# Kernel tuning notes

Measured on AMD Instinct MI355X. Metric: run time of the kernel, lower is better.

Reference implementation:

```python
import jax, jax.numpy as jnp
import numpy as np

B, DIM, H, W = 4, 512, 64, 64
HEADS = 8
MAX_FREQ = 10000.0


def _rope_cos_sin(h, w, head_dim, dtype):
    # 2D RoPE: first quarter of half_dim uses row position, second quarter uses col position
    half = head_dim // 2
    quarter = half // 2
    pos_h = jnp.arange(h, dtype=dtype)
    pos_w = jnp.arange(w, dtype=dtype)
    gh, gw = jnp.meshgrid(pos_h, pos_w, indexing='ij')
    pos = jnp.stack([gh.ravel(), gw.ravel()], axis=-1)  # [N, 2]
    freqs = 1.0 / (MAX_FREQ ** (jnp.arange(quarter, dtype=dtype) / quarter))  # [quarter]
    ang_x = pos[:, 0:1] * freqs  # [N, quarter]
    ang_y = pos[:, 1:2] * freqs  # [N, quarter]
    cos = jnp.concatenate([jnp.cos(ang_x), jnp.cos(ang_y)], axis=-1)  # [N, half]
    sin = jnp.concatenate([jnp.sin(ang_x), jnp.sin(ang_y)], axis=-1)  # [N, half]
    return cos, sin


def _apply_rope(x, cos, sin):
    # x: [B, heads, N, head_dim]; cos/sin: [N, head_dim//2]
    d = x.shape[-1] // 2
    x1, x2 = x[..., :d], x[..., d:]
    return jnp.concatenate([x1 * cos - x2 * sin, x1 * sin + x2 * cos], axis=-1)


def setup_inputs() -> dict:
    key = jax.random.key(0)
    kx, kq, kp = jax.random.split(key, 3)
    x = jax.random.normal(kx, (B, DIM, H, W), dtype=jnp.float32)
    w_qkv = jax.random.normal(kq, (3 * DIM, DIM), dtype=jnp.float32) * (DIM ** -0.5)
    w_proj = jax.random.normal(kp, (DIM, DIM), dtype=jnp.float32) * (DIM ** -0.5)
    return {"x": x, "w_qkv": w_qkv, "w_proj": w_proj}


def reference(x, w_qkv, w_proj):
    Bb, C, Hh, Ww = x.shape
    heads = HEADS
    hd = C // heads
    N = Hh * Ww
    # 1x1 conv (bias-free) == channel-wise linear
    qkv = jnp.einsum('bchw,oc->bohw', x, w_qkv)  # [B, 3C, H, W]
    qkv = qkv.reshape(Bb, 3, heads, hd, Hh, Ww).transpose(1, 0, 2, 4, 5, 3)  # [3, B, heads, H, W, hd]
    q = qkv[0].reshape(Bb, heads, N, hd)
    k = qkv[1].reshape(Bb, heads, N, hd)
    v = qkv[2].reshape(Bb, heads, N, hd)
    cos, sin = _rope_cos_sin(Hh, Ww, hd, x.dtype)
    q = _apply_rope(q, cos, sin)
    k = _apply_rope(k, cos, sin)
    scale = hd ** -0.5
    attn = jax.nn.softmax(jnp.einsum('bhnd,bhmd->bhnm', q, k) * scale, axis=-1)  # [B, heads, N, N]
    out = jnp.einsum('bhnm,bhmd->bhnd', attn, v)  # [B, heads, N, hd]
    out = out.reshape(Bb, heads, Hh, Ww, hd).transpose(0, 1, 4, 2, 3).reshape(Bb, C, Hh, Ww)
    return jnp.einsum('bchw,oc->bohw', out, w_proj)
```

## Files before the change

### kernel.cpp

```cpp
#include <hip/hip_runtime.h>
#include <math.h>

#define B_    4
#define CDIM  512
#define HEADS 8
#define HD    64
#define NN    4096
#define QSZ   ((size_t)B_*HEADS*NN*HD)
#define SCALE_Q 0.18033688011112042f

typedef __attribute__((ext_vector_type(8))) short short8;
typedef __attribute__((ext_vector_type(4))) float f32x4;
union U4S8 { uint4 u; short8 s; };

__device__ inline unsigned pk(float a, float b) {
    unsigned ua = __float_as_uint(a), ub = __float_as_uint(b);
    ua += 0x7FFFu + ((ua >> 16) & 1u);
    ub += 0x7FFFu + ((ub >> 16) & 1u);
    return (ua >> 16) | (ub & 0xFFFF0000u);
}
__device__ inline unsigned short bf16_1(float a) {
    unsigned ua = __float_as_uint(a);
    ua += 0x7FFFu + ((ua >> 16) & 1u);
    return (unsigned short)(ua >> 16);
}
__device__ inline unsigned pkru(float a, float b) {
    unsigned ua = __float_as_uint(a) + 0x8000u;
    unsigned ub = __float_as_uint(b) + 0x8000u;
    return __builtin_amdgcn_perm(ub, ua, 0x07060302);
}

__device__ inline void load_lds16(const unsigned short* g, unsigned short* l) {
    __builtin_amdgcn_global_load_lds(
        (const __attribute__((address_space(1))) unsigned int*)g,
        (__attribute__((address_space(3))) unsigned int*)l, 16, 0, 0);
}

__global__ void conv_w_kernel(const float* __restrict__ wq, const float* __restrict__ wp,
                              unsigned short* __restrict__ wqb, unsigned short* __restrict__ wpb) {
    int id = blockIdx.x * 256 + threadIdx.x;
    const float* src; unsigned short* dst; size_t off; float sc = 1.0f;
    if (id < 98304) { src = wq; dst = wqb; off = (size_t)id * 8; if (off < 262144) sc = SCALE_Q; }
    else            { src = wp; dst = wpb; off = (size_t)(id - 98304) * 8; }
    float4 a = *(const float4*)(src + off);
    float4 b = *(const float4*)(src + off + 4);
    uint4 u;
    u.x = pk(a.x * sc, a.y * sc); u.y = pk(a.z * sc, a.w * sc);
    u.z = pk(b.x * sc, b.y * sc); u.w = pk(b.z * sc, b.w * sc);
    *(uint4*)(dst + off) = u;
}

__global__ void rope_table_kernel(float* __restrict__ ct, float* __restrict__ st) {
    int id = blockIdx.x * 256 + threadIdx.x;
    int j = id >> 12, n = id & 4095;
    int i = j & 15;
    float pos = (j < 16) ? (float)(n >> 6) : (float)(n & 63);
    float freq = exp2f(-(float)i * 0.8304820237218406f);
    float ang = pos * freq;
    ct[id] = cosf(ang);
    st[id] = sinf(ang);
}

__global__ __launch_bounds__(256) void transpose_x_kernel(
        const float* __restrict__ x, unsigned short* __restrict__ xt) {
    __shared__ unsigned short T[64 * 72];
    int t = threadIdx.x;
    int b = blockIdx.z, c0 = blockIdx.y * 64, n0 = blockIdx.x * 64;
    const float* xb = x + ((size_t)b * CDIM + c0) * NN + n0;
    int crow = t >> 2, nseg = t & 3;
#pragma unroll
    for (int g = 0; g < 4; ++g) {
        float4 f = *(const float4*)(xb + (size_t)crow * NN + nseg * 16 + g * 4);
        int nb = nseg * 16 + g * 4;
        T[(nb + 0) * 72 + crow] = bf16_1(f.x);
        T[(nb + 1) * 72 + crow] = bf16_1(f.y);
        T[(nb + 2) * 72 + crow] = bf16_1(f.z);
        T[(nb + 3) * 72 + crow] = bf16_1(f.w);
    }
    __syncthreads();
    unsigned short* xo = xt + ((size_t)b * NN + n0) * CDIM + c0;
    int nrow = t >> 2, cseg = t & 3;
    uint4 u0 = *(uint4*)(T + nrow * 72 + cseg * 16);
    uint4 u1 = *(uint4*)(T + nrow * 72 + cseg * 16 + 8);
    *(uint4*)(xo + (size_t)nrow * CDIM + cseg * 16)     = u0;
    *(uint4*)(xo + (size_t)nrow * CDIM + cseg * 16 + 8) = u1;
}

__global__ __launch_bounds__(256, 2) void qkv_mfma_kernel(
        const unsigned short* __restrict__ xt, const unsigned short* __restrict__ wq,
        unsigned short* __restrict__ qbf, unsigned short* __restrict__ kbf,
        unsigned short* __restrict__ vt,
        const float* __restrict__ ct, const float* __restrict__ st) {
    __shared__ unsigned short smem[8192];
    int t = threadIdx.x;
    int lane = t & 63, w = t >> 6;
    int qlo = lane & 15, quad = lane >> 4;
    int b = blockIdx.z, o0 = blockIdx.y * 128, n0 = blockIdx.x * 128;
    const unsigned short* xb = xt + (size_t)b * NN * CDIM;
    int row = t >> 2, seg = t & 3;
    int wn = (w & 1) * 64, wo = (w >> 1) * 64;

    f32x4 acc[4][4];
#pragma unroll
    for (int i = 0; i < 4; ++i)
#pragma unroll
        for (int j = 0; j < 4; ++j) acc[i][j] = f32x4{0.f, 0.f, 0.f, 0.f};

    for (int k0 = 0; k0 < 512; k0 += 32) {
        __syncthreads();
        load_lds16(xb + (size_t)(n0 + row) * 512 + k0 + seg * 8,        smem + t * 8);
        load_lds16(xb + (size_t)(n0 + 64 + row) * 512 + k0 + seg * 8,   smem + 2048 + t * 8);
        load_lds16(wq + (size_t)(o0 + row) * 512 + k0 + seg * 8,        smem + 4096 + t * 8);
        load_lds16(wq + (size_t)(o0 + 64 + row) * 512 + k0 + seg * 8,   smem + 6144 + t * 8);
        __syncthreads();
        U4S8 af[4], bf[4];
#pragma unroll
        for (int mt = 0; mt < 4; ++mt)
            af[mt].u = *(const uint4*)(smem + (wn + 16 * mt + qlo) * 32 + quad * 8);
#pragma unroll
        for (int nt = 0; nt < 4; ++nt)
            bf[nt].u = *(const uint4*)(smem + 4096 + (wo + 16 * nt + qlo) * 32 + quad * 8);
#pragma unroll
        for (int mt = 0; mt < 4; ++mt)
#pragma unroll
            for (int nt = 0; nt < 4; ++nt)
                acc[mt][nt] = __builtin_amdgcn_mfma_f32_16x16x32_bf16(
                    af[mt].s, bf[nt].s, acc[mt][nt], 0, 0, 0);
    }

    int og = o0 + wo;
    int s = og >> 9;
    int h = (og & 511) >> 6;
    int bh = b * HEADS + h;
    if (s < 2) {
        unsigned short* dst = (s ? kbf : qbf) + (size_t)bh * NN * HD;
#pragma unroll
        for (int mt = 0; mt < 4; ++mt) {
            int nbase = n0 + wn + 16 * mt + 4 * quad;
#pragma unroll
            for (int ntp = 0; ntp < 2; ++ntp) {
                int j = 16 * ntp + qlo;
                float4 c4 = *(const float4*)(ct + (size_t)j * NN + nbase);
                float4 s4 = *(const float4*)(st + (size_t)j * NN + nbase);
                float cc[4] = {c4.x, c4.y, c4.z, c4.w};
                float ss[4] = {s4.x, s4.y, s4.z, s4.w};
#pragma unroll
                for (int r = 0; r < 4; ++r) {
                    float x1 = acc[mt][ntp][r], x2 = acc[mt][ntp + 2][r];
                    size_t base = (size_t)(nbase + r) * HD;
                    dst[base + j]      = bf16_1(x1 * cc[r] - x2 * ss[r]);
                    dst[base + j + 32] = bf16_1(x1 * ss[r] + x2 * cc[r]);
                }
            }
        }
    } else {
        unsigned short* dst = vt + (size_t)bh * HD * NN;
#pragma unroll
        for (int mt = 0; mt < 4; ++mt)
#pragma unroll
            for (int nt = 0; nt < 4; ++nt) {
                int d = 16 * nt + qlo;
                int n = n0 + wn + 16 * mt + 4 * quad;
                uint2 u;
                u.x = pk(acc[mt][nt][0], acc[mt][nt][1]);
                u.y = pk(acc[mt][nt][2], acc[mt][nt][3]);
                *(uint2*)(dst + (size_t)d * NN + n) = u;
            }
    }
}

__global__ __launch_bounds__(256, 2) void attn_kernel(
        const unsigned short* __restrict__ qbf, const unsigned short* __restrict__ kbf,
        const unsigned short* __restrict__ vt, unsigned short* __restrict__ aot) {
    __shared__ unsigned char smem[18432];
    int t = threadIdx.x;
    int lane = t & 63, w = t >> 6;
    int qlo = lane & 15, quad = lane >> 4;
    int bb = blockIdx.z, hh = blockIdx.y;
    int bh = bb * HEADS + hh;
    int n0w = blockIdx.x * 256 + w * 64;

    U4S8 qf[4][2];
    const unsigned short* qg = qbf + ((size_t)bh * NN + n0w) * HD;
#pragma unroll
    for (int nt = 0; nt < 4; ++nt)
#pragma unroll
        for (int kt = 0; kt < 2; ++kt)
            qf[nt][kt].u = *(const uint4*)(qg + (size_t)(16 * nt + qlo) * 64 + 32 * kt + 8 * quad);

    f32x4 O[4][4];
#pragma unroll
    for (int mt = 0; mt < 4; ++mt)
#pragma unroll
        for (int nt = 0; nt < 4; ++nt) O[mt][nt] = f32x4{0.f, 0.f, 0.f, 0.f};
    float lx[4] = {0.f, 0.f, 0.f, 0.f};
    float ly[4] = {0.f, 0.f, 0.f, 0.f};

    const uint4* kg = (const uint4*)kbf + (size_t)bh * NN * 8;
    const uint4* vg = (const uint4*)vt  + (size_t)bh * 64 * 512;

    int rr0 = t >> 3, s8 = t & 7;
    int voff = (s8 >> 2) * 64 + (s8 & 1) * 32 + ((s8 >> 1) & 1) * 8;
    uint4 kr0, kr1, vr0, vr1;
    kr0 = kg[(size_t)rr0 * 8 + s8];
    kr1 = kg[(size_t)(32 + rr0) * 8 + s8];
    vr0 = vg[(size_t)rr0 * 512 + s8];
    vr1 = vg[(size_t)(32 + rr0) * 512 + s8];

    for (int c = 0; c < NN / 64; ++c) {
        __syncthreads();
        *(uint4*)(smem + rr0 * 144 + s8 * 16)        = kr0;
        *(uint4*)(smem + (32 + rr0) * 144 + s8 * 16) = kr1;
        *(uint2*)(smem + 9216 + rr0 * 144 + voff)            = make_uint2(vr0.x, vr0.y);
        *(uint2*)(smem + 9216 + rr0 * 144 + voff + 16)       = make_uint2(vr0.z, vr0.w);
        *(uint2*)(smem + 9216 + (32 + rr0) * 144 + voff)     = make_uint2(vr1.x, vr1.y);
        *(uint2*)(smem + 9216 + (32 + rr0) * 144 + voff + 16)= make_uint2(vr1.z, vr1.w);
        __syncthreads();
        if (c + 1 < NN / 64) {
            int m0 = (c + 1) * 64;
            kr0 = kg[(size_t)(m0 + rr0) * 8 + s8];
            kr1 = kg[(size_t)(m0 + 32 + rr0) * 8 + s8];
            vr0 = vg[(size_t)rr0 * 512 + (m0 >> 3) + s8];
            vr1 = vg[(size_t)(32 + rr0) * 512 + (m0 >> 3) + s8];
        }

        f32x4 S[4][4];
#pragma unroll
        for (int mt = 0; mt < 4; ++mt)
#pragma unroll
            for (int nt = 0; nt < 4; ++nt) S[mt][nt] = f32x4{0.f, 0.f, 0.f, 0.f};
#pragma unroll
        for (int kt = 0; kt < 2; ++kt) {
            U4S8 ka[4];
#pragma unroll
            for (int mt = 0; mt < 4; ++mt)
                ka[mt].u = *(const uint4*)(smem + (16 * mt + qlo) * 144 + kt * 64 + quad * 16);
#pragma unroll
            for (int nt = 0; nt < 4; ++nt)
#pragma unroll
                for (int mt = 0; mt < 4; ++mt)
                    S[mt][nt] = __builtin_amdgcn_mfma_f32_16x16x32_bf16(
                        ka[mt].s, qf[nt][kt].s, S[mt][nt], 0, 0, 0);
        }

        uint2 pd[4][4];
#pragma unroll
        for (int nt = 0; nt < 4; ++nt)
#pragma unroll
            for (int mt = 0; mt < 4; ++mt) {
                f32x4 s4 = S[mt][nt];
                float p0 = __builtin_amdgcn_exp2f(s4[0]);
                float p1 = __builtin_amdgcn_exp2f(s4[1]);
                float p2 = __builtin_amdgcn_exp2f(s4[2]);
                float p3 = __builtin_amdgcn_exp2f(s4[3]);
                lx[nt] += p0 + p2;
                ly[nt] += p1 + p3;
                pd[nt][mt] = make_uint2(pkru(p0, p1), pkru(p2, p3));
            }

#pragma unroll
        for (int kt = 0; kt < 2; ++kt) {
            U4S8 pa[4];
#pragma unroll
            for (int mtP = 0; mtP < 4; ++mtP)
                pa[mtP].u = make_uint4(pd[mtP][2 * kt].x, pd[mtP][2 * kt].y,
                                       pd[mtP][2 * kt + 1].x, pd[mtP][2 * kt + 1].y);
#pragma unroll
            for (int nt = 0; nt < 4; ++nt) {
                U4S8 vb;
                vb.u = *(const uint4*)(smem + 9216 + (16 * nt + qlo) * 144 + kt * 64 + quad * 16);
#pragma unroll
                for (int mtP = 0; mtP < 4; ++mtP)
                    O[mtP][nt] = __builtin_amdgcn_mfma_f32_16x16x32_bf16(
                        pa[mtP].s, vb.s, O[mtP][nt], 0, 0, 0);
            }
        }
    }

    float linv[4];
#pragma unroll
    for (int nt = 0; nt < 4; ++nt) {
        float l = lx[nt] + ly[nt];
        l += __shfl_xor(l, 16, 64);
        l += __shfl_xor(l, 32, 64);
        linv[nt] = 1.0f / l;
    }
    __syncthreads();
    unsigned short* Tw = (unsigned short*)(smem + w * 4608);
    unsigned short* aob = aot + ((size_t)bb * NN) * CDIM + hh * 64;
#pragma unroll
    for (int mt = 0; mt < 4; ++mt) {
        float iv[4];
#pragma unroll
        for (int r = 0; r < 4; ++r) iv[r] = __shfl(linv[mt], 4 * quad + r, 64);
#pragma unroll
        for (int nt = 0; nt < 4; ++nt)
#pragma unroll
            for (int r = 0; r < 4; ++r)
                Tw[(4 * quad + r) * 72 + 16 * nt + qlo] = bf16_1(O[mt][nt][r] * iv[r]);
        int row = lane >> 2, cseg = lane & 3;
        uint4 u0 = *(uint4*)(Tw + row * 72 + cseg * 16);
        uint4 u1 = *(uint4*)(Tw + row * 72 + cseg * 16 + 8);
        unsigned short* arow = aob + (size_t)(n0w + 16 * mt + row) * CDIM + cseg * 16;
        *(uint4*)(arow)     = u0;
        *(uint4*)(arow + 8) = u1;
    }
}

__global__ __launch_bounds__(256, 2) void proj_mfma_kernel(
        const unsigned short* __restrict__ aot, const unsigned short* __restrict__ wp,
        float* __restrict__ out) {
    __shared__ unsigned short smem[8192];
    int t = threadIdx.x;
    int lane = t & 63, w = t >> 6;
    int qlo = lane & 15, quad = lane >> 4;
    int b = blockIdx.z, o0 = blockIdx.y * 128, n0 = blockIdx.x * 128;
    const unsigned short* ab = aot + (size_t)b * NN * CDIM;
    int row = t >> 2, seg = t & 3;
    int wn = (w & 1) * 64, wo = (w >> 1) * 64;

    f32x4 acc[4][4];
#pragma unroll
    for (int i = 0; i < 4; ++i)
#pragma unroll
        for (int j = 0; j < 4; ++j) acc[i][j] = f32x4{0.f, 0.f, 0.f, 0.f};

    for (int k0 = 0; k0 < 512; k0 += 32) {
        __syncthreads();
        load_lds16(ab + (size_t)(n0 + row) * 512 + k0 + seg * 8,        smem + t * 8);
        load_lds16(ab + (size_t)(n0 + 64 + row) * 512 + k0 + seg * 8,   smem + 2048 + t * 8);
        load_lds16(wp + (size_t)(o0 + row) * 512 + k0 + seg * 8,        smem + 4096 + t * 8);
        load_lds16(wp + (size_t)(o0 + 64 + row) * 512 + k0 + seg * 8,   smem + 6144 + t * 8);
        __syncthreads();
        U4S8 af[4], bf[4];
#pragma unroll
        for (int mt = 0; mt < 4; ++mt)
            af[mt].u = *(const uint4*)(smem + (wn + 16 * mt + qlo) * 32 + quad * 8);
#pragma unroll
        for (int nt = 0; nt < 4; ++nt)
            bf[nt].u = *(const uint4*)(smem + 4096 + (wo + 16 * nt + qlo) * 32 + quad * 8);
#pragma unroll
        for (int mt = 0; mt < 4; ++mt)
#pragma unroll
            for (int nt = 0; nt < 4; ++nt)
                acc[mt][nt] = __builtin_amdgcn_mfma_f32_16x16x32_bf16(
                    af[mt].s, bf[nt].s, acc[mt][nt], 0, 0, 0);
    }

    float* ob = out + (size_t)b * CDIM * NN;
#pragma unroll
    for (int mt = 0; mt < 4; ++mt)
#pragma unroll
        for (int nt = 0; nt < 4; ++nt) {
            int o = o0 + wo + 16 * nt + qlo;
            int n = n0 + wn + 16 * mt + 4 * quad;
            *(float4*)(ob + (size_t)o * NN + n) = *(float4*)&acc[mt][nt];
        }
}

extern "C" void kernel_launch(void* const* d_in, const int* in_sizes, int n_in,
                              void* d_out, int out_size, void* d_ws, size_t ws_size,
                              hipStream_t stream) {
    const float* x      = (const float*)d_in[0];
    const float* w_qkv  = (const float*)d_in[1];
    const float* w_proj = (const float*)d_in[2];
    float* out = (float*)d_out;
    unsigned short* ws = (unsigned short*)d_ws;

    unsigned short* xt  = ws;
    unsigned short* qbf = xt  + QSZ;
    unsigned short* kbf = qbf + QSZ;
    unsigned short* vt  = kbf + QSZ;
    unsigned short* aot = vt  + QSZ;
    unsigned short* wqb = aot + QSZ;
    unsigned short* wpb = wqb + 786432;
    float* ct = (float*)(wpb + 262144);
    float* st = ct + 32 * 4096;

    conv_w_kernel<<<512, 256, 0, stream>>>(w_qkv, w_proj, wqb, wpb);
    rope_table_kernel<<<512, 256, 0, stream>>>(ct, st);
    transpose_x_kernel<<<dim3(64, 8, B_), 256, 0, stream>>>(x, xt);
    qkv_mfma_kernel<<<dim3(32, 12, B_), 256, 0, stream>>>(xt, wqb, qbf, kbf, vt, ct, st);
    attn_kernel<<<dim3(NN / 256, HEADS, B_), 256, 0, stream>>>(qbf, kbf, vt, aot);
    proj_mfma_kernel<<<dim3(32, 4, B_), 256, 0, stream>>>(aot, wpb, out);
}
```

Before: 291.6 us.

## Rewrite attention inner loop with 32x32x16 MFMA, 128-key tiles and MFMA row sums

The attention kernel switches from 16x16x32 to 32x32x16 bf16 MFMA tiles and stages 128 keys per iteration instead of 64, which halves the number of barriers. The softmax denominator is now accumulated by an extra MFMA against a ones vector rather than scalar adds and cross-lane shuffles. The grid becomes 1D with a remapped block index so that blocks sharing the same head are scheduled close together, which may improve L2 reuse of K and V. In exchange, LDS use roughly doubles, register pressure rises from the 16-wide accumulators, and the extra MFMAs for the row sums add matrix-unit work.

```diff
diff --git a/kernel.cpp b/kernel.cpp
--- a/kernel.cpp
+++ b/kernel.cpp
@@ -11,6 +11,7 @@
 
 typedef __attribute__((ext_vector_type(8))) short short8;
 typedef __attribute__((ext_vector_type(4))) float f32x4;
+typedef __attribute__((ext_vector_type(16))) float f32x16;
 union U4S8 { uint4 u; short8 s; };
 
 __device__ inline unsigned pk(float a, float b) {
@@ -172,138 +173,135 @@
 __global__ __launch_bounds__(256, 2) void attn_kernel(
         const unsigned short* __restrict__ qbf, const unsigned short* __restrict__ kbf,
         const unsigned short* __restrict__ vt, unsigned short* __restrict__ aot) {
-    __shared__ unsigned char smem[18432];
+    __shared__ unsigned char smem[35840];
+    const int VB = 18432;
     int t = threadIdx.x;
     int lane = t & 63, w = t >> 6;
-    int qlo = lane & 15, quad = lane >> 4;
-    int bb = blockIdx.z, hh = blockIdx.y;
-    int bh = bb * HEADS + hh;
-    int n0w = blockIdx.x * 256 + w * 64;
-
-    U4S8 qf[4][2];
+    int lo5 = lane & 31, h = lane >> 5;
+    int L = blockIdx.x;
+    int bh = (L & 7) + 8 * (L >> 7);
+    int qb = (L >> 3) & 15;
+    int bb = bh >> 3, hh = bh & 7;
+    int n0w = qb * 256 + w * 64;
+
+    U4S8 qf[2][4];
     const unsigned short* qg = qbf + ((size_t)bh * NN + n0w) * HD;
 #pragma unroll
-    for (int nt = 0; nt < 4; ++nt)
-#pragma unroll
-        for (int kt = 0; kt < 2; ++kt)
-            qf[nt][kt].u = *(const uint4*)(qg + (size_t)(16 * nt + qlo) * 64 + 32 * kt + 8 * quad);
-
-    f32x4 O[4][4];
-#pragma unroll
-    for (int mt = 0; mt < 4; ++mt)
-#pragma unroll
-        for (int nt = 0; nt < 4; ++nt) O[mt][nt] = f32x4{0.f, 0.f, 0.f, 0.f};
-    float lx[4] = {0.f, 0.f, 0.f, 0.f};
-    float ly[4] = {0.f, 0.f, 0.f, 0.f};
+    for (int qt = 0; qt < 2; ++qt)
+#pragma unroll
+        for (int kt = 0; kt < 4; ++kt)
+            qf[qt][kt].u = *(const uint4*)(qg + (size_t)(32 * qt + lo5) * 64 + kt * 16 + 8 * h);
+
+    f32x16 O[2][2], lac[2];
+#pragma unroll
+    for (int i = 0; i < 16; ++i) {
+        O[0][0][i] = 0.f; O[0][1][i] = 0.f; O[1][0][i] = 0.f; O[1][1][i] = 0.f;
+        lac[0][i] = 0.f; lac[1][i] = 0.f;
+    }
+    U4S8 ones;
+    ones.u = make_uint4(0x3F803F80u, 0x3F803F80u, 0x3F803F80u, 0x3F803F80u);
 
     const uint4* kg = (const uint4*)kbf + (size_t)bh * NN * 8;
     const uint4* vg = (const uint4*)vt  + (size_t)bh * 64 * 512;
 
-    int rr0 = t >> 3, s8 = t & 7;
-    int voff = (s8 >> 2) * 64 + (s8 & 1) * 32 + ((s8 >> 1) & 1) * 8;
-    uint4 kr0, kr1, vr0, vr1;
-    kr0 = kg[(size_t)rr0 * 8 + s8];
-    kr1 = kg[(size_t)(32 + rr0) * 8 + s8];
-    vr0 = vg[(size_t)rr0 * 512 + s8];
-    vr1 = vg[(size_t)(32 + rr0) * 512 + s8];
-
-    for (int c = 0; c < NN / 64; ++c) {
-        __syncthreads();
-        *(uint4*)(smem + rr0 * 144 + s8 * 16)        = kr0;
-        *(uint4*)(smem + (32 + rr0) * 144 + s8 * 16) = kr1;
-        *(uint2*)(smem + 9216 + rr0 * 144 + voff)            = make_uint2(vr0.x, vr0.y);
-        *(uint2*)(smem + 9216 + rr0 * 144 + voff + 16)       = make_uint2(vr0.z, vr0.w);
-        *(uint2*)(smem + 9216 + (32 + rr0) * 144 + voff)     = make_uint2(vr1.x, vr1.y);
-        *(uint2*)(smem + 9216 + (32 + rr0) * 144 + voff + 16)= make_uint2(vr1.z, vr1.w);
-        __syncthreads();
-        if (c + 1 < NN / 64) {
-            int m0 = (c + 1) * 64;
-            kr0 = kg[(size_t)(m0 + rr0) * 8 + s8];
-            kr1 = kg[(size_t)(m0 + 32 + rr0) * 8 + s8];
-            vr0 = vg[(size_t)rr0 * 512 + (m0 >> 3) + s8];
-            vr1 = vg[(size_t)(32 + rr0) * 512 + (m0 >> 3) + s8];
-        }
-
-        f32x4 S[4][4];
-#pragma unroll
-        for (int mt = 0; mt < 4; ++mt)
-#pragma unroll
-            for (int nt = 0; nt < 4; ++nt) S[mt][nt] = f32x4{0.f, 0.f, 0.f, 0.f};
-#pragma unroll
-        for (int kt = 0; kt < 2; ++kt) {
-            U4S8 ka[4];
-#pragma unroll
-            for (int mt = 0; mt < 4; ++mt)
-                ka[mt].u = *(const uint4*)(smem + (16 * mt + qlo) * 144 + kt * 64 + quad * 16);
-#pragma unroll
-            for (int nt = 0; nt < 4; ++nt)
-#pragma unroll
-                for (int mt = 0; mt < 4; ++mt)
-                    S[mt][nt] = __builtin_amdgcn_mfma_f32_16x16x32_bf16(
-                        ka[mt].s, qf[nt][kt].s, S[mt][nt], 0, 0, 0);
-        }
-
-        uint2 pd[4][4];
-#pragma unroll
-        for (int nt = 0; nt < 4; ++nt)
-#pragma unroll
-            for (int mt = 0; mt < 4; ++mt) {
-                f32x4 s4 = S[mt][nt];
-                float p0 = __builtin_amdgcn_exp2f(s4[0]);
-                float p1 = __builtin_amdgcn_exp2f(s4[1]);
-                float p2 = __builtin_amdgcn_exp2f(s4[2]);
-                float p3 = __builtin_amdgcn_exp2f(s4[3]);
-                lx[nt] += p0 + p2;
-                ly[nt] += p1 + p3;
-                pd[nt][mt] = make_uint2(pkru(p0, p1), pkru(p2, p3));
-            }
-
-#pragma unroll
-        for (int kt = 0; kt < 2; ++kt) {
-            U4S8 pa[4];
-#pragma unroll
-            for (int mtP = 0; mtP < 4; ++mtP)
-                pa[mtP].u = make_uint4(pd[mtP][2 * kt].x, pd[mtP][2 * kt].y,
-                                       pd[mtP][2 * kt + 1].x, pd[mtP][2 * kt + 1].y);
-#pragma unroll
-            for (int nt = 0; nt < 4; ++nt) {
-                U4S8 vb;
-                vb.u = *(const uint4*)(smem + 9216 + (16 * nt + qlo) * 144 + kt * 64 + quad * 16);
-#pragma unroll
-                for (int mtP = 0; mtP < 4; ++mtP)
-                    O[mtP][nt] = __builtin_amdgcn_mfma_f32_16x16x32_bf16(
-                        pa[mtP].s, vb.s, O[mtP][nt], 0, 0, 0);
-            }
-        }
-    }
-
-    float linv[4];
-#pragma unroll
-    for (int nt = 0; nt < 4; ++nt) {
-        float l = lx[nt] + ly[nt];
-        l += __shfl_xor(l, 16, 64);
-        l += __shfl_xor(l, 32, 64);
-        linv[nt] = 1.0f / l;
-    }
+    int kof[4], vof[4];
+    const uint4* kgp[4]; const uint4* vgp[4];
+    uint4 kr[4], vr[4];
+#pragma unroll
+    for (int i = 0; i < 4; ++i) {
+        int idx = t + 256 * i;
+        kof[i] = (idx >> 3) * 144 + (idx & 7) * 16;
+        kgp[i] = kg + (size_t)(idx >> 3) * 8 + (idx & 7);
+        int hd = idx >> 4, u = idx & 15;
+        vof[i] = VB + hd * 272 + 32 * (u >> 1) + 8 * (u & 1);
+        vgp[i] = vg + (size_t)hd * 512 + u;
+        kr[i] = kgp[i][0];
+        vr[i] = vgp[i][0];
+    }
+
+    for (int it = 0; it < 32; ++it) {
+        __syncthreads();
+#pragma unroll
+        for (int i = 0; i < 4; ++i)
+            *(uint4*)(smem + kof[i]) = kr[i];
+#pragma unroll
+        for (int i = 0; i < 4; ++i) {
+            *(uint2*)(smem + vof[i])      = make_uint2(vr[i].x, vr[i].y);
+            *(uint2*)(smem + vof[i] + 16) = make_uint2(vr[i].z, vr[i].w);
+        }
+        __syncthreads();
+        if (it + 1 < 32) {
+#pragma unroll
+            for (int i = 0; i < 4; ++i) {
+                kr[i] = kgp[i][(size_t)(it + 1) * 1024];
+                vr[i] = vgp[i][(size_t)(it + 1) * 16];
+            }
+        }
+
+#pragma unroll
+        for (int sc = 0; sc < 2; ++sc) {
+            U4S8 pa[2][4];
+#pragma unroll
+            for (int mt = 0; mt < 2; ++mt) {
+                f32x16 S0 = {0.f,0.f,0.f,0.f,0.f,0.f,0.f,0.f,0.f,0.f,0.f,0.f,0.f,0.f,0.f,0.f};
+                f32x16 S1 = {0.f,0.f,0.f,0.f,0.f,0.f,0.f,0.f,0.f,0.f,0.f,0.f,0.f,0.f,0.f,0.f};
+                int kbase = 9216 * sc + 4608 * mt + lo5 * 144 + 16 * h;
+#pragma unroll
+                for (int kt = 0; kt < 4; ++kt) {
+                    U4S8 ka;
+                    ka.u = *(const uint4*)(smem + kbase + kt * 32);
+                    S0 = __builtin_amdgcn_mfma_f32_32x32x16_bf16(ka.s, qf[0][kt].s, S0, 0, 0, 0);
+                    S1 = __builtin_amdgcn_mfma_f32_32x32x16_bf16(ka.s, qf[1][kt].s, S1, 0, 0, 0);
+                }
+#pragma unroll
+                for (int gg = 0; gg < 2; ++gg) {
+                    int rb = 8 * gg;
+                    pa[0][2 * mt + gg].u = make_uint4(
+                        pkru(__builtin_amdgcn_exp2f(S0[rb + 0]), __builtin_amdgcn_exp2f(S0[rb + 1])),
+                        pkru(__builtin_amdgcn_exp2f(S0[rb + 2]), __builtin_amdgcn_exp2f(S0[rb + 3])),
+                        pkru(__builtin_amdgcn_exp2f(S0[rb + 4]), __builtin_amdgcn_exp2f(S0[rb + 5])),
+                        pkru(__builtin_amdgcn_exp2f(S0[rb + 6]), __builtin_amdgcn_exp2f(S0[rb + 7])));
+                    pa[1][2 * mt + gg].u = make_uint4(
+                        pkru(__builtin_amdgcn_exp2f(S1[rb + 0]), __builtin_amdgcn_exp2f(S1[rb + 1])),
+                        pkru(__builtin_amdgcn_exp2f(S1[rb + 2]), __builtin_amdgcn_exp2f(S1[rb + 3])),
+                        pkru(__builtin_amdgcn_exp2f(S1[rb + 4]), __builtin_amdgcn_exp2f(S1[rb + 5])),
+                        pkru(__builtin_amdgcn_exp2f(S1[rb + 6]), __builtin_amdgcn_exp2f(S1[rb + 7])));
+                }
+            }
+            int vbase = VB + lo5 * 272 + 16 * h + 128 * sc;
+#pragma unroll
+            for (int g = 0; g < 4; ++g) {
+                U4S8 vb0, vb1;
+                vb0.u = *(const uint4*)(smem + vbase + 32 * g);
+                vb1.u = *(const uint4*)(smem + vbase + 8704 + 32 * g);
+                lac[0]  = __builtin_amdgcn_mfma_f32_32x32x16_bf16(pa[0][g].s, ones.s, lac[0], 0, 0, 0);
+                lac[1]  = __builtin_amdgcn_mfma_f32_32x32x16_bf16(pa[1][g].s, ones.s, lac[1], 0, 0, 0);
+                O[0][0] = __builtin_amdgcn_mfma_f32_32x32x16_bf16(pa[0][g].s, vb0.s, O[0][0], 0, 0, 0);
+                O[0][1] = __builtin_amdgcn_mfma_f32_32x32x16_bf16(pa[0][g].s, vb1.s, O[0][1], 0, 0, 0);
+                O[1][0] = __builtin_amdgcn_mfma_f32_32x32x16_bf16(pa[1][g].s, vb0.s, O[1][0], 0, 0, 0);
+                O[1][1] = __builtin_amdgcn_mfma_f32_32x32x16_bf16(pa[1][g].s, vb1.s, O[1][1], 0, 0, 0);
+            }
+        }
+    }
+
     __syncthreads();
     unsigned short* Tw = (unsigned short*)(smem + w * 4608);
-    unsigned short* aob = aot + ((size_t)bb * NN) * CDIM + hh * 64;
-#pragma unroll
-    for (int mt = 0; mt < 4; ++mt) {
-        float iv[4];
-#pragma unroll
-        for (int r = 0; r < 4; ++r) iv[r] = __shfl(linv[mt], 4 * quad + r, 64);
-#pragma unroll
-        for (int nt = 0; nt < 4; ++nt)
-#pragma unroll
-            for (int r = 0; r < 4; ++r)
-                Tw[(4 * quad + r) * 72 + 16 * nt + qlo] = bf16_1(O[mt][nt][r] * iv[r]);
-        int row = lane >> 2, cseg = lane & 3;
-        uint4 u0 = *(uint4*)(Tw + row * 72 + cseg * 16);
-        uint4 u1 = *(uint4*)(Tw + row * 72 + cseg * 16 + 8);
-        unsigned short* arow = aob + (size_t)(n0w + 16 * mt + row) * CDIM + cseg * 16;
-        *(uint4*)(arow)     = u0;
-        *(uint4*)(arow + 8) = u1;
+    unsigned short* aob = aot + (size_t)bb * NN * CDIM + hh * 64;
+#pragma unroll
+    for (int qt = 0; qt < 2; ++qt) {
+#pragma unroll
+        for (int r = 0; r < 16; ++r) {
+            int qrow = (r & 3) + 8 * (r >> 2) + 4 * h;
+            float inv = __builtin_amdgcn_rcpf(lac[qt][r]);
+            Tw[qrow * 68 + lo5]      = bf16_1(O[qt][0][r] * inv);
+            Tw[qrow * 68 + 32 + lo5] = bf16_1(O[qt][1][r] * inv);
+        }
+        unsigned short* arow = aob + (size_t)(n0w + 32 * qt + (lane >> 1)) * CDIM + (lane & 1) * 8;
+#pragma unroll
+        for (int rep = 0; rep < 4; ++rep) {
+            uint4 u = *(const uint4*)(Tw + (lane >> 1) * 68 + (lane & 1) * 8 + rep * 16);
+            *(uint4*)(arow + rep * 16) = u;
+        }
     }
 }
 
@@ -381,6 +379,6 @@
     rope_table_kernel<<<512, 256, 0, stream>>>(ct, st);
     transpose_x_kernel<<<dim3(64, 8, B_), 256, 0, stream>>>(x, xt);
     qkv_mfma_kernel<<<dim3(32, 12, B_), 256, 0, stream>>>(xt, wqb, qbf, kbf, vt, ct, st);
-    attn_kernel<<<dim3(NN / 256, HEADS, B_), 256, 0, stream>>>(qbf, kbf, vt, aot);
+    attn_kernel<<<512, 256, 0, stream>>>(qbf, kbf, vt, aot);
     proj_mfma_kernel<<<dim3(32, 4, B_), 256, 0, stream>>>(aot, wpb, out);
 }
```

Result: slower. 319.1 us (+9.4%).

## Halve attention query tile per block and remap grid for more blocks

Applied to the files above, without the earlier changes.

The attention kernel now gives each block 128 queries (32 per wave) instead of 256, which doubles the grid to 1024 blocks, and raises the launch-bounds occupancy hint from 2 to 3. A 1D grid mapping interleaves heads so neighbouring blocks cover different (batch, head) pairs. The aim is more blocks and waves in flight on the GPU's many CUs, with lower register pressure per wave. In exchange each K/V tile loaded into shared memory is reused by half as many queries, so K/V traffic doubles.

```diff
diff --git a/kernel.cpp b/kernel.cpp
--- a/kernel.cpp
+++ b/kernel.cpp
@@ -169,32 +169,34 @@
     }
 }
 
-__global__ __launch_bounds__(256, 2) void attn_kernel(
+__global__ __launch_bounds__(256, 3) void attn_kernel(
         const unsigned short* __restrict__ qbf, const unsigned short* __restrict__ kbf,
         const unsigned short* __restrict__ vt, unsigned short* __restrict__ aot) {
     __shared__ unsigned char smem[18432];
     int t = threadIdx.x;
     int lane = t & 63, w = t >> 6;
     int qlo = lane & 15, quad = lane >> 4;
-    int bb = blockIdx.z, hh = blockIdx.y;
-    int bh = bb * HEADS + hh;
-    int n0w = blockIdx.x * 256 + w * 64;
-
-    U4S8 qf[4][2];
+    int L = blockIdx.x;
+    int bh = (L & 7) + 8 * (L >> 8);
+    int qb = (L >> 3) & 31;
+    int bb = bh >> 3, hh = bh & 7;
+    int n0w = qb * 128 + w * 32;
+
+    U4S8 qf[2][2];
     const unsigned short* qg = qbf + ((size_t)bh * NN + n0w) * HD;
 #pragma unroll
-    for (int nt = 0; nt < 4; ++nt)
+    for (int qt = 0; qt < 2; ++qt)
 #pragma unroll
         for (int kt = 0; kt < 2; ++kt)
-            qf[nt][kt].u = *(const uint4*)(qg + (size_t)(16 * nt + qlo) * 64 + 32 * kt + 8 * quad);
-
-    f32x4 O[4][4];
-#pragma unroll
-    for (int mt = 0; mt < 4; ++mt)
-#pragma unroll
-        for (int nt = 0; nt < 4; ++nt) O[mt][nt] = f32x4{0.f, 0.f, 0.f, 0.f};
-    float lx[4] = {0.f, 0.f, 0.f, 0.f};
-    float ly[4] = {0.f, 0.f, 0.f, 0.f};
+            qf[qt][kt].u = *(const uint4*)(qg + (size_t)(16 * qt + qlo) * 64 + 32 * kt + 8 * quad);
+
+    f32x4 O[2][4];
+#pragma unroll
+    for (int i = 0; i < 2; ++i)
+#pragma unroll
+        for (int j = 0; j < 4; ++j) O[i][j] = f32x4{0.f, 0.f, 0.f, 0.f};
+    float lx[2] = {0.f, 0.f};
+    float ly[2] = {0.f, 0.f};
 
     const uint4* kg = (const uint4*)kbf + (size_t)bh * NN * 8;
     const uint4* vg = (const uint4*)vt  + (size_t)bh * 64 * 512;
@@ -211,10 +213,10 @@
         __syncthreads();
         *(uint4*)(smem + rr0 * 144 + s8 * 16)        = kr0;
         *(uint4*)(smem + (32 + rr0) * 144 + s8 * 16) = kr1;
-        *(uint2*)(smem + 9216 + rr0 * 144 + voff)            = make_uint2(vr0.x, vr0.y);
-        *(uint2*)(smem + 9216 + rr0 * 144 + voff + 16)       = make_uint2(vr0.z, vr0.w);
-        *(uint2*)(smem + 9216 + (32 + rr0) * 144 + voff)     = make_uint2(vr1.x, vr1.y);
-        *(uint2*)(smem + 9216 + (32 + rr0) * 144 + voff + 16)= make_uint2(vr1.z, vr1.w);
+        *(uint2*)(smem + 9216 + rr0 * 144 + voff)             = make_uint2(vr0.x, vr0.y);
+        *(uint2*)(smem + 9216 + rr0 * 144 + voff + 16)        = make_uint2(vr0.z, vr0.w);
+        *(uint2*)(smem + 9216 + (32 + rr0) * 144 + voff)      = make_uint2(vr1.x, vr1.y);
+        *(uint2*)(smem + 9216 + (32 + rr0) * 144 + voff + 16) = make_uint2(vr1.z, vr1.w);
         __syncthreads();
         if (c + 1 < NN / 64) {
             int m0 = (c + 1) * 64;
@@ -224,11 +226,11 @@
             vr1 = vg[(size_t)(32 + rr0) * 512 + (m0 >> 3) + s8];
         }
 
-        f32x4 S[4][4];
-#pragma unroll
-        for (int mt = 0; mt < 4; ++mt)
-#pragma unroll
-            for (int nt = 0; nt < 4; ++nt) S[mt][nt] = f32x4{0.f, 0.f, 0.f, 0.f};
+        f32x4 S[4][2];
+#pragma unroll
+        for (int mt = 0; mt < 4; ++mt)
+#pragma unroll
+            for (int qt = 0; qt < 2; ++qt) S[mt][qt] = f32x4{0.f, 0.f, 0.f, 0.f};
 #pragma unroll
         for (int kt = 0; kt < 2; ++kt) {
             U4S8 ka[4];
@@ -236,72 +238,72 @@
             for (int mt = 0; mt < 4; ++mt)
                 ka[mt].u = *(const uint4*)(smem + (16 * mt + qlo) * 144 + kt * 64 + quad * 16);
 #pragma unroll
-            for (int nt = 0; nt < 4; ++nt)
+            for (int qt = 0; qt < 2; ++qt)
 #pragma unroll
                 for (int mt = 0; mt < 4; ++mt)
-                    S[mt][nt] = __builtin_amdgcn_mfma_f32_16x16x32_bf16(
-                        ka[mt].s, qf[nt][kt].s, S[mt][nt], 0, 0, 0);
-        }
-
-        uint2 pd[4][4];
-#pragma unroll
-        for (int nt = 0; nt < 4; ++nt)
+                    S[mt][qt] = __builtin_amdgcn_mfma_f32_16x16x32_bf16(
+                        ka[mt].s, qf[qt][kt].s, S[mt][qt], 0, 0, 0);
+        }
+
+        uint2 pd[2][4];
+#pragma unroll
+        for (int qt = 0; qt < 2; ++qt)
 #pragma unroll
             for (int mt = 0; mt < 4; ++mt) {
-                f32x4 s4 = S[mt][nt];
+                f32x4 s4 = S[mt][qt];
                 float p0 = __builtin_amdgcn_exp2f(s4[0]);
                 float p1 = __builtin_amdgcn_exp2f(s4[1]);
                 float p2 = __builtin_amdgcn_exp2f(s4[2]);
                 float p3 = __builtin_amdgcn_exp2f(s4[3]);
-                lx[nt] += p0 + p2;
-                ly[nt] += p1 + p3;
-                pd[nt][mt] = make_uint2(pkru(p0, p1), pkru(p2, p3));
+                lx[qt] += p0 + p2;
+                ly[qt] += p1 + p3;
+                pd[qt][mt] = make_uint2(pkru(p0, p1), pkru(p2, p3));
             }
 
 #pragma unroll
         for (int kt = 0; kt < 2; ++kt) {
-            U4S8 pa[4];
-#pragma unroll
-            for (int mtP = 0; mtP < 4; ++mtP)
-                pa[mtP].u = make_uint4(pd[mtP][2 * kt].x, pd[mtP][2 * kt].y,
-                                       pd[mtP][2 * kt + 1].x, pd[mtP][2 * kt + 1].y);
-#pragma unroll
-            for (int nt = 0; nt < 4; ++nt) {
+            U4S8 pa[2];
+#pragma unroll
+            for (int qt = 0; qt < 2; ++qt)
+                pa[qt].u = make_uint4(pd[qt][2 * kt].x, pd[qt][2 * kt].y,
+                                      pd[qt][2 * kt + 1].x, pd[qt][2 * kt + 1].y);
+#pragma unroll
+            for (int ht = 0; ht < 4; ++ht) {
                 U4S8 vb;
-                vb.u = *(const uint4*)(smem + 9216 + (16 * nt + qlo) * 144 + kt * 64 + quad * 16);
-#pragma unroll
-                for (int mtP = 0; mtP < 4; ++mtP)
-                    O[mtP][nt] = __builtin_amdgcn_mfma_f32_16x16x32_bf16(
-                        pa[mtP].s, vb.s, O[mtP][nt], 0, 0, 0);
+                vb.u = *(const uint4*)(smem + 9216 + (16 * ht + qlo) * 144 + kt * 64 + quad * 16);
+#pragma unroll
+                for (int qt = 0; qt < 2; ++qt)
+                    O[qt][ht] = __builtin_amdgcn_mfma_f32_16x16x32_bf16(
+                        pa[qt].s, vb.s, O[qt][ht], 0, 0, 0);
             }
         }
     }
 
-    float linv[4];
-#pragma unroll
-    for (int nt = 0; nt < 4; ++nt) {
-        float l = lx[nt] + ly[nt];
+    float linv[2];
+#pragma unroll
+    for (int qt = 0; qt < 2; ++qt) {
+        float l = lx[qt] + ly[qt];
         l += __shfl_xor(l, 16, 64);
         l += __shfl_xor(l, 32, 64);
-        linv[nt] = 1.0f / l;
+        linv[qt] = 1.0f / l;
     }
     __syncthreads();
     unsigned short* Tw = (unsigned short*)(smem + w * 4608);
-    unsigned short* aob = aot + ((size_t)bb * NN) * CDIM + hh * 64;
-#pragma unroll
-    for (int mt = 0; mt < 4; ++mt) {
+    unsigned short* aob = aot + (size_t)bb * NN * CDIM + hh * 64;
+#pragma unroll
+    for (int qt = 0; qt < 2; ++qt) {
         float iv[4];
 #pragma unroll
-        for (int r = 0; r < 4; ++r) iv[r] = __shfl(linv[mt], 4 * quad + r, 64);
-#pragma unroll
-        for (int nt = 0; nt < 4; ++nt)
+        for (int r = 0; r < 4; ++r) iv[r] = __shfl(linv[qt], 4 * quad + r, 64);
+#pragma unroll
+        for (int ht = 0; ht < 4; ++ht)
 #pragma unroll
             for (int r = 0; r < 4; ++r)
-                Tw[(4 * quad + r) * 72 + 16 * nt + qlo] = bf16_1(O[mt][nt][r] * iv[r]);
+                Tw[(4 * quad + r) * 72 + 16 * ht + qlo] = bf16_1(O[qt][ht][r] * iv[r]);
         int row = lane >> 2, cseg = lane & 3;
         uint4 u0 = *(uint4*)(Tw + row * 72 + cseg * 16);
         uint4 u1 = *(uint4*)(Tw + row * 72 + cseg * 16 + 8);
-        unsigned short* arow = aob + (size_t)(n0w + 16 * mt + row) * CDIM + cseg * 16;
+        unsigned short* arow = aob + (size_t)(n0w + 16 * qt + row) * CDIM + cseg * 16;
         *(uint4*)(arow)     = u0;
         *(uint4*)(arow + 8) = u1;
     }
@@ -381,6 +383,6 @@
     rope_table_kernel<<<512, 256, 0, stream>>>(ct, st);
     transpose_x_kernel<<<dim3(64, 8, B_), 256, 0, stream>>>(x, xt);
     qkv_mfma_kernel<<<dim3(32, 12, B_), 256, 0, stream>>>(xt, wqb, qbf, kbf, vt, ct, st);
-    attn_kernel<<<dim3(NN / 256, HEADS, B_), 256, 0, stream>>>(qbf, kbf, vt, aot);
+    attn_kernel<<<1024, 256, 0, stream>>>(qbf, kbf, vt, aot);
     proj_mfma_kernel<<<dim3(32, 4, B_), 256, 0, stream>>>(aot, wpb, out);
 }
```

Measured after the change: 302.0 us. +3.6%, slower.

## Double attention KV chunk to 128 keys and remap block order for locality

Applied to the files above, without the earlier changes.

The attention kernel now stages 128 keys and values per iteration instead of 64, halving the number of barrier pairs and loop iterations, with each thread loading four 16-byte K and V segments. The launch becomes a 1D grid whose index is remapped so that the eight heads, and then query blocks, are spread in an order meant to improve L2 reuse of K/V. Shared memory grows to about 35 KB and register pressure rises from the larger prefetch buffers, which could reduce occupancy below two blocks per CU.

```diff
diff --git a/kernel.cpp b/kernel.cpp
--- a/kernel.cpp
+++ b/kernel.cpp
@@ -172,13 +172,16 @@
 __global__ __launch_bounds__(256, 2) void attn_kernel(
         const unsigned short* __restrict__ qbf, const unsigned short* __restrict__ kbf,
         const unsigned short* __restrict__ vt, unsigned short* __restrict__ aot) {
-    __shared__ unsigned char smem[18432];
+    __shared__ unsigned char smem[35840];
+    const int VB = 18432;
     int t = threadIdx.x;
     int lane = t & 63, w = t >> 6;
     int qlo = lane & 15, quad = lane >> 4;
-    int bb = blockIdx.z, hh = blockIdx.y;
-    int bh = bb * HEADS + hh;
-    int n0w = blockIdx.x * 256 + w * 64;
+    int L = blockIdx.x;
+    int bh = (L & 7) + 8 * (L >> 7);
+    int qb = (L >> 3) & 15;
+    int bb = bh >> 3, hh = bh & 7;
+    int n0w = qb * 256 + w * 64;
 
     U4S8 qf[4][2];
     const unsigned short* qg = qbf + ((size_t)bh * NN + n0w) * HD;
@@ -199,80 +202,96 @@
     const uint4* kg = (const uint4*)kbf + (size_t)bh * NN * 8;
     const uint4* vg = (const uint4*)vt  + (size_t)bh * 64 * 512;
 
-    int rr0 = t >> 3, s8 = t & 7;
-    int voff = (s8 >> 2) * 64 + (s8 & 1) * 32 + ((s8 >> 1) & 1) * 8;
-    uint4 kr0, kr1, vr0, vr1;
-    kr0 = kg[(size_t)rr0 * 8 + s8];
-    kr1 = kg[(size_t)(32 + rr0) * 8 + s8];
-    vr0 = vg[(size_t)rr0 * 512 + s8];
-    vr1 = vg[(size_t)(32 + rr0) * 512 + s8];
-
-    for (int c = 0; c < NN / 64; ++c) {
-        __syncthreads();
-        *(uint4*)(smem + rr0 * 144 + s8 * 16)        = kr0;
-        *(uint4*)(smem + (32 + rr0) * 144 + s8 * 16) = kr1;
-        *(uint2*)(smem + 9216 + rr0 * 144 + voff)            = make_uint2(vr0.x, vr0.y);
-        *(uint2*)(smem + 9216 + rr0 * 144 + voff + 16)       = make_uint2(vr0.z, vr0.w);
-        *(uint2*)(smem + 9216 + (32 + rr0) * 144 + voff)     = make_uint2(vr1.x, vr1.y);
-        *(uint2*)(smem + 9216 + (32 + rr0) * 144 + voff + 16)= make_uint2(vr1.z, vr1.w);
-        __syncthreads();
-        if (c + 1 < NN / 64) {
-            int m0 = (c + 1) * 64;
-            kr0 = kg[(size_t)(m0 + rr0) * 8 + s8];
-            kr1 = kg[(size_t)(m0 + 32 + rr0) * 8 + s8];
-            vr0 = vg[(size_t)rr0 * 512 + (m0 >> 3) + s8];
-            vr1 = vg[(size_t)(32 + rr0) * 512 + (m0 >> 3) + s8];
+    int kof[4], vof[4];
+    const uint4* kgp[4]; const uint4* vgp[4];
+    uint4 kr[4], vr[4];
+#pragma unroll
+    for (int i = 0; i < 4; ++i) {
+        int idx = t + 256 * i;
+        kof[i] = (idx >> 3) * 144 + (idx & 7) * 16;
+        kgp[i] = kg + (size_t)(idx >> 3) * 8 + (idx & 7);
+        int hd = idx >> 4, u = idx & 15;
+        int sc = u >> 3, s8 = u & 7;
+        vof[i] = VB + hd * 272 + sc * 128
+               + (s8 >> 2) * 64 + (s8 & 1) * 32 + ((s8 >> 1) & 1) * 8;
+        vgp[i] = vg + (size_t)hd * 512 + u;
+        kr[i] = kgp[i][0];
+        vr[i] = vgp[i][0];
+    }
+
+    for (int it = 0; it < 32; ++it) {
+        __syncthreads();
+#pragma unroll
+        for (int i = 0; i < 4; ++i)
+            *(uint4*)(smem + kof[i]) = kr[i];
+#pragma unroll
+        for (int i = 0; i < 4; ++i) {
+            *(uint2*)(smem + vof[i])      = make_uint2(vr[i].x, vr[i].y);
+            *(uint2*)(smem + vof[i] + 16) = make_uint2(vr[i].z, vr[i].w);
         }
-
-        f32x4 S[4][4];
-#pragma unroll
-        for (int mt = 0; mt < 4; ++mt)
-#pragma unroll
-            for (int nt = 0; nt < 4; ++nt) S[mt][nt] = f32x4{0.f, 0.f, 0.f, 0.f};
-#pragma unroll
-        for (int kt = 0; kt < 2; ++kt) {
-            U4S8 ka[4];
+        __syncthreads();
+        if (it + 1 < 32) {
+#pragma unroll
+            for (int i = 0; i < 4; ++i) {
+                kr[i] = kgp[i][(size_t)(it + 1) * 1024];
+                vr[i] = vgp[i][(size_t)(it + 1) * 16];
+            }
+        }
+
+#pragma unroll
+        for (int sc2 = 0; sc2 < 2; ++sc2) {
+            f32x4 S[4][4];
 #pragma unroll
             for (int mt = 0; mt < 4; ++mt)
-                ka[mt].u = *(const uint4*)(smem + (16 * mt + qlo) * 144 + kt * 64 + quad * 16);
+#pragma unroll
+                for (int nt = 0; nt < 4; ++nt) S[mt][nt] = f32x4{0.f, 0.f, 0.f, 0.f};
+#pragma unroll
+            for (int kt = 0; kt < 2; ++kt) {
+                U4S8 ka[4];
+#pragma unroll
+                for (int mt = 0; mt < 4; ++mt)
+                    ka[mt].u = *(const uint4*)(smem + (64 * sc2 + 16 * mt + qlo) * 144
+                                               + kt * 64 + quad * 16);
+#pragma unroll
+                for (int nt = 0; nt < 4; ++nt)
+#pragma unroll
+                    for (int mt = 0; mt < 4; ++mt)
+                        S[mt][nt] = __builtin_amdgcn_mfma_f32_16x16x32_bf16(
+                            ka[mt].s, qf[nt][kt].s, S[mt][nt], 0, 0, 0);
+            }
+
+            uint2 pd[4][4];
 #pragma unroll
             for (int nt = 0; nt < 4; ++nt)
 #pragma unroll
-                for (int mt = 0; mt < 4; ++mt)
-                    S[mt][nt] = __builtin_amdgcn_mfma_f32_16x16x32_bf16(
-                        ka[mt].s, qf[nt][kt].s, S[mt][nt], 0, 0, 0);
-        }
-
-        uint2 pd[4][4];
-#pragma unroll
-        for (int nt = 0; nt < 4; ++nt)
-#pragma unroll
-            for (int mt = 0; mt < 4; ++mt) {
-                f32x4 s4 = S[mt][nt];
-                float p0 = __builtin_amdgcn_exp2f(s4[0]);
-                float p1 = __builtin_amdgcn_exp2f(s4[1]);
-                float p2 = __builtin_amdgcn_exp2f(s4[2]);
-                float p3 = __builtin_amdgcn_exp2f(s4[3]);
-                lx[nt] += p0 + p2;
-                ly[nt] += p1 + p3;
-                pd[nt][mt] = make_uint2(pkru(p0, p1), pkru(p2, p3));
-            }
-
-#pragma unroll
-        for (int kt = 0; kt < 2; ++kt) {
-            U4S8 pa[4];
-#pragma unroll
-            for (int mtP = 0; mtP < 4; ++mtP)
-                pa[mtP].u = make_uint4(pd[mtP][2 * kt].x, pd[mtP][2 * kt].y,
-                                       pd[mtP][2 * kt + 1].x, pd[mtP][2 * kt + 1].y);
-#pragma unroll
-            for (int nt = 0; nt < 4; ++nt) {
-                U4S8 vb;
-                vb.u = *(const uint4*)(smem + 9216 + (16 * nt + qlo) * 144 + kt * 64 + quad * 16);
+                for (int mt = 0; mt < 4; ++mt) {
+                    f32x4 s4 = S[mt][nt];
+                    float p0 = __builtin_amdgcn_exp2f(s4[0]);
+                    float p1 = __builtin_amdgcn_exp2f(s4[1]);
+                    float p2 = __builtin_amdgcn_exp2f(s4[2]);
+                    float p3 = __builtin_amdgcn_exp2f(s4[3]);
+                    lx[nt] += p0 + p2;
+                    ly[nt] += p1 + p3;
+                    pd[nt][mt] = make_uint2(pkru(p0, p1), pkru(p2, p3));
+                }
+
+#pragma unroll
+            for (int kt = 0; kt < 2; ++kt) {
+                U4S8 pa[4];
 #pragma unroll
                 for (int mtP = 0; mtP < 4; ++mtP)
-                    O[mtP][nt] = __builtin_amdgcn_mfma_f32_16x16x32_bf16(
-                        pa[mtP].s, vb.s, O[mtP][nt], 0, 0, 0);
+                    pa[mtP].u = make_uint4(pd[mtP][2 * kt].x, pd[mtP][2 * kt].y,
+                                           pd[mtP][2 * kt + 1].x, pd[mtP][2 * kt + 1].y);
+#pragma unroll
+                for (int nt = 0; nt < 4; ++nt) {
+                    U4S8 vb;
+                    vb.u = *(const uint4*)(smem + VB + (16 * nt + qlo) * 272
+                                           + sc2 * 128 + kt * 64 + quad * 16);
+#pragma unroll
+                    for (int mtP = 0; mtP < 4; ++mtP)
+                        O[mtP][nt] = __builtin_amdgcn_mfma_f32_16x16x32_bf16(
+                            pa[mtP].s, vb.s, O[mtP][nt], 0, 0, 0);
+                }
             }
         }
     }
@@ -287,7 +306,7 @@
     }
     __syncthreads();
     unsigned short* Tw = (unsigned short*)(smem + w * 4608);
-    unsigned short* aob = aot + ((size_t)bb * NN) * CDIM + hh * 64;
+    unsigned short* aob = aot + (size_t)bb * NN * CDIM + hh * 64;
 #pragma unroll
     for (int mt = 0; mt < 4; ++mt) {
         float iv[4];
@@ -381,6 +400,6 @@
     rope_table_kernel<<<512, 256, 0, stream>>>(ct, st);
     transpose_x_kernel<<<dim3(64, 8, B_), 256, 0, stream>>>(x, xt);
     qkv_mfma_kernel<<<dim3(32, 12, B_), 256, 0, stream>>>(xt, wqb, qbf, kbf, vt, ct, st);
-    attn_kernel<<<dim3(NN / 256, HEADS, B_), 256, 0, stream>>>(qbf, kbf, vt, aot);
+    attn_kernel<<<512, 256, 0, stream>>>(qbf, kbf, vt, aot);
     proj_mfma_kernel<<<dim3(32, 4, B_), 256, 0, stream>>>(aot, wpb, out);
 }
```

Result: slower. 484.7 us (+66.2%).
